# Kernel tuning notes

Hardware: AMD Instinct MI355X
Metric: run time of the kernel (lower is better)

Reference implementation:

```python
import jax, jax.numpy as jnp
import numpy as np

NUM_FEATURES = 5
HIDDEN = 64
NUM_CLASSES = 5
N_NODES = 100000
N_EDGES = 1600000


def setup_inputs() -> dict:
    key = jax.random.key(0)
    ks = jax.random.split(key, 8)
    x = jax.random.normal(ks[0], (N_NODES, 4, NUM_FEATURES), dtype=jnp.float32)
    edge_index = jax.random.randint(ks[1], (2, N_EDGES), 0, N_NODES, dtype=jnp.int64)
    batch = jnp.zeros((N_NODES,), dtype=jnp.int64)
    # GCNConv layer 1: 5 -> 64, layer 2: 64 -> 64, output Linear: 64 -> 5
    W1 = jax.random.normal(ks[2], (NUM_FEATURES, HIDDEN), dtype=jnp.float32) / np.sqrt(NUM_FEATURES)
    b1 = jnp.zeros((HIDDEN,), dtype=jnp.float32)
    W2 = jax.random.normal(ks[3], (HIDDEN, HIDDEN), dtype=jnp.float32) / np.sqrt(HIDDEN)
    b2 = jnp.zeros((HIDDEN,), dtype=jnp.float32)
    Wout = jax.random.normal(ks[4], (HIDDEN, NUM_CLASSES), dtype=jnp.float32) / np.sqrt(HIDDEN)
    bout = jnp.zeros((NUM_CLASSES,), dtype=jnp.float32)
    return {"x": x, "edge_index": edge_index, "batch": batch,
            "W1": W1, "b1": b1, "W2": W2, "b2": b2, "Wout": Wout, "bout": bout}


def reference(x, edge_index, batch, W1, b1, W2, b2, Wout, bout):
    N = x.shape[0]
    src, dst = edge_index[0], edge_index[1]
    # GCN symmetric normalization with self-loops: deg counts incoming edges + self loop
    deg = jax.ops.segment_sum(jnp.ones(src.shape, jnp.float32), dst, num_segments=N) + 1.0
    dinv_sqrt = jax.lax.rsqrt(deg)
    norm = dinv_sqrt[src] * dinv_sqrt[dst]            # [E]
    self_norm = (1.0 / deg)[:, None]                  # self-loop weight deg^-1

    def gcn_conv(h, W, b):
        h = h @ W                                     # [N, out]
        agg = jax.ops.segment_sum(h[src] * norm[:, None], dst, num_segments=N)
        return agg + h * self_norm + b

    h = jax.nn.relu(gcn_conv(x[:, -1, :], W1, b1))    # [N, HIDDEN]
    h = jax.nn.relu(gcn_conv(h, W2, b2))              # [N, HIDDEN]
    return jax.nn.softmax(h @ Wout + bout, axis=1)    # [N, 5]
```

## Files before the change

### kernel.cpp

```cpp
#include <hip/hip_runtime.h>
#include <hip/hip_fp16.h>

#define HID 64
#define NF 5
#define NC 5

#define WSH 9
#define WINN 512
#define NBMAX 256
#define SRCB 17
#define NBLK 256


__global__ __launch_bounds__(512) void k_bcount(const int* __restrict__ dst, int E, int chunk,
                                                int nb, int* __restrict__ cntmat) {
    __shared__ int cnt[NBMAX];
    int t = threadIdx.x;
    for (int i = t; i < nb; i += 512) cnt[i] = 0;
    __syncthreads();
    int c0 = blockIdx.x * chunk;
    int c1 = c0 + chunk; if (c1 > E) c1 = E;
    for (int i = c0 + t; i < c1; i += 512)
        atomicAdd(&cnt[dst[i] >> WSH], 1);
    __syncthreads();
    for (int i = t; i < nb; i += 512) cntmat[blockIdx.x * nb + i] = cnt[i];
}

__global__ __launch_bounds__(NBLK) void k_wscan(int* __restrict__ cntmat, int nb,
                                                int* __restrict__ btot) {
    __shared__ int s[NBLK];
    int b = blockIdx.x;
    int t = threadIdx.x;
    int v = cntmat[t * nb + b];
    s[t] = v;
    __syncthreads();
    for (int o = 1; o < NBLK; o <<= 1) {
        int u = (t >= o) ? s[t - o] : 0;
        __syncthreads();
        s[t] += u;
        __syncthreads();
    }
    cntmat[t * nb + b] = s[t] - v;
    if (t == NBLK - 1) btot[b] = s[t];
}

__global__ __launch_bounds__(256) void k_bscan2(const int* __restrict__ btot, int nb, int N,
                                                int* __restrict__ bbase,
                                                int* __restrict__ offsets) {
    __shared__ int s[256];
    int t = threadIdx.x;
    int v = (t < nb) ? btot[t] : 0;
    s[t] = v;
    __syncthreads();
    for (int o = 1; o < 256; o <<= 1) {
        int u = (t >= o) ? s[t - o] : 0;
        __syncthreads();
        s[t] += u;
        __syncthreads();
    }
    if (t < nb) bbase[t] = s[t] - v;
    if (t == nb - 1) { bbase[nb] = s[t]; offsets[N] = s[t]; }
}

__global__ __launch_bounds__(512) void k_bfill(const int* __restrict__ src,
                                               const int* __restrict__ dst, int E, int chunk,
                                               int nb, const int* __restrict__ bbase,
                                               const int* __restrict__ cntmat,
                                               unsigned int* __restrict__ pairbuf) {
    __shared__ int wcur[NBMAX];
    int t = threadIdx.x;
    int blk = blockIdx.x;
    for (int i = t; i < nb; i += 512)
        wcur[i] = bbase[i] + cntmat[blk * nb + i];
    __syncthreads();
    int c0 = blk * chunk;
    int c1 = c0 + chunk; if (c1 > E) c1 = E;
    for (int i = c0 + t; i < c1; i += 512) {
        int d = dst[i];
        int b = d >> WSH;
        int p = atomicAdd(&wcur[b], 1);
        pairbuf[p] = ((unsigned)(d & (WINN - 1)) << SRCB) | (unsigned)src[i];
    }
}

__global__ __launch_bounds__(WINN) void k_csr(const unsigned int* __restrict__ pairbuf,
                                              const int* __restrict__ bbase, int N,
                                              const float* __restrict__ x,
                                              int* __restrict__ offsets,
                                              int* __restrict__ csr_src,
                                              float* __restrict__ dinv,
                                              float* __restrict__ xs8) {
    int b = blockIdx.x, t = threadIdx.x;
    int winStart = b << WSH;
    int rbeg = bbase[b], rend = bbase[b + 1];
    __shared__ int deg[WINN];
    __shared__ int cur[WINN];
    __shared__ int s[WINN];
    deg[t] = 0;
    __syncthreads();
    for (int p = rbeg + t; p < rend; p += WINN)
        atomicAdd(&deg[pairbuf[p] >> SRCB], 1);
    __syncthreads();
    int v = deg[t];
    s[t] = v;
    __syncthreads();
    for (int o = 1; o < WINN; o <<= 1) {
        int u = (t >= o) ? s[t - o] : 0;
        __syncthreads();
        s[t] += u;
        __syncthreads();
    }
    int node = winStart + t;
    if (node < N) {
        int base = rbeg + s[t] - v;
        offsets[node] = base;
        cur[t] = base;
        float dv = rsqrtf((float)v + 1.0f);
        dinv[node] = dv;
        const float* xr = x + (size_t)node * (4 * NF) + 3 * NF;
        float4 v0, v1;
        v0.x = xr[0] * dv; v0.y = xr[1] * dv; v0.z = xr[2] * dv; v0.w = xr[3] * dv;
        v1.x = xr[4] * dv; v1.y = 0.f; v1.z = 0.f; v1.w = 0.f;
        float4* xp = reinterpret_cast<float4*>(xs8 + (size_t)node * 8);
        xp[0] = v0;
        xp[1] = v1;
    }
    __syncthreads();
    for (int p = rbeg + t; p < rend; p += WINN) {
        unsigned u = pairbuf[p];
        int dl = u >> SRCB;
        int sn = u & ((1u << SRCB) - 1);
        int pos = atomicAdd(&cur[dl], 1);
        csr_src[pos] = sn;
    }
}


__global__ __launch_bounds__(256) void k_aggX(const float* __restrict__ xs8,
                                              const float* __restrict__ W1,
                                              const int* __restrict__ offsets,
                                              const int* __restrict__ csr_src,
                                              const float* __restrict__ dinv,
                                              const float* __restrict__ b1,
                                              __half* __restrict__ g1, int N) {
    int wid = (blockIdx.x * blockDim.x + threadIdx.x) >> 6;
    int lane = threadIdx.x & 63;
    int g = lane >> 1;
    int h = lane & 1;
    float w0 = W1[0 * HID + lane], w1 = W1[1 * HID + lane], w2 = W1[2 * HID + lane],
          w3 = W1[3 * HID + lane], w4 = W1[4 * HID + lane];
    if (wid >= N) return;
    int e0 = offsets[wid], e1 = offsets[wid + 1];
    float4 acc = {0.f, 0.f, 0.f, 0.f};
    int ee = e0 + g;
    int s = (ee < e1) ? csr_src[ee] : -1;
    for (int e = e0; e < e1; e += 32) {
        int cs = s;
        int en = e + 32 + g;
        s = (en < e1) ? csr_src[en] : -1;
        bool p = (cs >= 0);
        int csc = p ? cs : 0;
        float4 v = *reinterpret_cast<const float4*>(xs8 + (size_t)csc * 8 + (h << 2));
        if (p) { acc.x += v.x; acc.y += v.y; acc.z += v.z; acc.w += v.w; }
    }
    if (g == 0) {
        float4 v = *reinterpret_cast<const float4*>(xs8 + (size_t)wid * 8 + (h << 2));
        acc.x += v.x; acc.y += v.y; acc.z += v.z; acc.w += v.w;
    }
#pragma unroll
    for (int o = 2; o < 64; o <<= 1) {
        acc.x += __shfl_xor(acc.x, o, 64);
        acc.y += __shfl_xor(acc.y, o, 64);
        acc.z += __shfl_xor(acc.z, o, 64);
        acc.w += __shfl_xor(acc.w, o, 64);
    }
    float a0 = __shfl(acc.x, 0, 2), a1 = __shfl(acc.y, 0, 2),
          a2 = __shfl(acc.z, 0, 2), a3 = __shfl(acc.w, 0, 2),
          a4 = __shfl(acc.x, 1, 2);
    float dv = dinv[wid];
    float sres = a0 * w0 + a1 * w1 + a2 * w2 + a3 * w3 + a4 * w4;
    float r = fmaxf(fmaf(dv, sres, b1[lane]), 0.f) * dv;
    g1[(size_t)wid * HID + lane] = __float2half(r);
}

__global__ __launch_bounds__(256) void k_aggG(const __half* __restrict__ g1,
                                              const int* __restrict__ offsets,
                                              const int* __restrict__ csr_src,
                                              const float* __restrict__ dinv,
                                              float* __restrict__ aggH, int N) {
    int wid = (blockIdx.x * blockDim.x + threadIdx.x) >> 6;
    if (wid >= N) return;
    int lane = threadIdx.x & 63;
    int g = lane >> 3;
    int f8 = (lane & 7) << 3;
    int e0 = offsets[wid], e1 = offsets[wid + 1];
    float acc[8];
#pragma unroll
    for (int i = 0; i < 8; ++i) acc[i] = 0.f;
    int ee = e0 + g;
    int s0 = (ee < e1) ? csr_src[ee] : -1;
    int s1 = (ee + 8 < e1) ? csr_src[ee + 8] : -1;
    for (int e = e0; e < e1; e += 16) {
        int cs0 = s0, cs1 = s1;
        int en0 = e + 16 + g, en1 = e + 24 + g;
        s0 = (en0 < e1) ? csr_src[en0] : -1;
        s1 = (en1 < e1) ? csr_src[en1] : -1;
        bool p0 = (cs0 >= 0), p1 = (cs1 >= 0);
        int c0 = p0 ? cs0 : 0, c1 = p1 ? cs1 : 0;
        float4 raw0 = *reinterpret_cast<const float4*>(g1 + (size_t)c0 * HID + f8);
        float4 raw1 = *reinterpret_cast<const float4*>(g1 + (size_t)c1 * HID + f8);
        if (p0) {
            float2 q0 = __half22float2(*reinterpret_cast<__half2*>(&raw0.x));
            float2 q1 = __half22float2(*reinterpret_cast<__half2*>(&raw0.y));
            float2 q2 = __half22float2(*reinterpret_cast<__half2*>(&raw0.z));
            float2 q3 = __half22float2(*reinterpret_cast<__half2*>(&raw0.w));
            acc[0] += q0.x; acc[1] += q0.y; acc[2] += q1.x; acc[3] += q1.y;
            acc[4] += q2.x; acc[5] += q2.y; acc[6] += q3.x; acc[7] += q3.y;
        }
        if (p1) {
            float2 q0 = __half22float2(*reinterpret_cast<__half2*>(&raw1.x));
            float2 q1 = __half22float2(*reinterpret_cast<__half2*>(&raw1.y));
            float2 q2 = __half22float2(*reinterpret_cast<__half2*>(&raw1.z));
            float2 q3 = __half22float2(*reinterpret_cast<__half2*>(&raw1.w));
            acc[0] += q0.x; acc[1] += q0.y; acc[2] += q1.x; acc[3] += q1.y;
            acc[4] += q2.x; acc[5] += q2.y; acc[6] += q3.x; acc[7] += q3.y;
        }
    }
#pragma unroll
    for (int o = 8; o < 64; o <<= 1) {
#pragma unroll
        for (int i = 0; i < 8; ++i) acc[i] += __shfl_xor(acc[i], o, 64);
    }
    if (lane < 8) {
        float4 raw = *reinterpret_cast<const float4*>(g1 + (size_t)wid * HID + f8);
        float2 q0 = __half22float2(*reinterpret_cast<__half2*>(&raw.x));
        float2 q1 = __half22float2(*reinterpret_cast<__half2*>(&raw.y));
        float2 q2 = __half22float2(*reinterpret_cast<__half2*>(&raw.z));
        float2 q3 = __half22float2(*reinterpret_cast<__half2*>(&raw.w));
        float dv = dinv[wid];
        float4 r0, r1;
        r0.x = dv * (acc[0] + q0.x); r0.y = dv * (acc[1] + q0.y);
        r0.z = dv * (acc[2] + q1.x); r0.w = dv * (acc[3] + q1.y);
        r1.x = dv * (acc[4] + q2.x); r1.y = dv * (acc[5] + q2.y);
        r1.z = dv * (acc[6] + q3.x); r1.w = dv * (acc[7] + q3.y);
        float4* dst4 = reinterpret_cast<float4*>(aggH + (size_t)wid * HID + f8);
        dst4[0] = r0;
        dst4[1] = r1;
    }
}

__global__ __launch_bounds__(256) void k_fuse(const float* __restrict__ aggH,
                                              const float* __restrict__ W2,
                                              const float* __restrict__ b2,
                                              const float* __restrict__ Wout,
                                              const float* __restrict__ bout,
                                              float* __restrict__ out, int N) {
    __shared__ float4 sh4[64][17];
    __shared__ float4 sW4[64 * 16];
    __shared__ float  swout[64][NC];
    __shared__ float  sb2[64];
    __shared__ float  sbout[8];
    int tx = threadIdx.x;
    int nb0 = blockIdx.x * 64;

    const float4* W2_4 = reinterpret_cast<const float4*>(W2);
    for (int i = tx; i < 64 * 16; i += 256) sW4[i] = W2_4[i];
    const float4* aggH4 = reinterpret_cast<const float4*>(aggH);
    for (int i = tx; i < 64 * 16; i += 256) {
        int row = i >> 4, c4 = i & 15;
        int node = nb0 + row;
        float4 v = {0.f, 0.f, 0.f, 0.f};
        if (node < N) v = aggH4[(size_t)node * 16 + c4];
        sh4[row][c4] = v;
    }
    if (tx < 64) sb2[tx] = b2[tx];
    for (int i = tx; i < 64 * NC; i += 256) swout[i / NC][i % NC] = Wout[i];
    if (tx < NC) sbout[tx] = bout[tx];
    __syncthreads();

    int ty = tx >> 4;
    int txl = tx & 15;

    float acc[4][4];
#pragma unroll
    for (int j = 0; j < 4; ++j)
#pragma unroll
        for (int i = 0; i < 4; ++i) acc[j][i] = 0.f;

    for (int k4 = 0; k4 < 16; ++k4) {
        float4 w0 = sW4[(k4 * 4 + 0) * 16 + txl];
        float4 w1 = sW4[(k4 * 4 + 1) * 16 + txl];
        float4 w2 = sW4[(k4 * 4 + 2) * 16 + txl];
        float4 w3 = sW4[(k4 * 4 + 3) * 16 + txl];
#pragma unroll
        for (int j = 0; j < 4; ++j) {
            float4 hq = sh4[ty * 4 + j][k4];
            acc[j][0] = fmaf(hq.x, w0.x, fmaf(hq.y, w1.x, fmaf(hq.z, w2.x, fmaf(hq.w, w3.x, acc[j][0]))));
            acc[j][1] = fmaf(hq.x, w0.y, fmaf(hq.y, w1.y, fmaf(hq.z, w2.y, fmaf(hq.w, w3.y, acc[j][1]))));
            acc[j][2] = fmaf(hq.x, w0.z, fmaf(hq.y, w1.z, fmaf(hq.z, w2.z, fmaf(hq.w, w3.z, acc[j][2]))));
            acc[j][3] = fmaf(hq.x, w0.w, fmaf(hq.y, w1.w, fmaf(hq.z, w2.w, fmaf(hq.w, w3.w, acc[j][3]))));
        }
    }

    float pl[4][NC];
#pragma unroll
    for (int j = 0; j < 4; ++j)
#pragma unroll
        for (int c = 0; c < NC; ++c) pl[j][c] = 0.f;
#pragma unroll
    for (int j = 0; j < 4; ++j) {
#pragma unroll
        for (int i = 0; i < 4; ++i) {
            int f = txl * 4 + i;
            float h2 = fmaxf(acc[j][i] + sb2[f], 0.f);
#pragma unroll
            for (int c = 0; c < NC; ++c) pl[j][c] = fmaf(h2, swout[f][c], pl[j][c]);
        }
    }
#pragma unroll
    for (int o = 1; o < 16; o <<= 1) {
#pragma unroll
        for (int j = 0; j < 4; ++j)
#pragma unroll
            for (int c = 0; c < NC; ++c) pl[j][c] += __shfl_xor(pl[j][c], o, 64);
    }
    if (txl == 0) {
#pragma unroll
        for (int j = 0; j < 4; ++j) {
            int node = nb0 + ty * 4 + j;
            if (node < N) {
                float lg[NC];
#pragma unroll
                for (int c = 0; c < NC; ++c) lg[c] = pl[j][c] + sbout[c];
                float m = lg[0];
#pragma unroll
                for (int c = 1; c < NC; ++c) m = fmaxf(m, lg[c]);
                float ssum = 0.f, ex[NC];
#pragma unroll
                for (int c = 0; c < NC; ++c) { ex[c] = __expf(lg[c] - m); ssum += ex[c]; }
                float inv = 1.0f / ssum;
#pragma unroll
                for (int c = 0; c < NC; ++c) out[(size_t)node * NC + c] = ex[c] * inv;
            }
        }
    }
}


extern "C" void kernel_launch(void* const* d_in, const int* in_sizes, int n_in,
                              void* d_out, int out_size, void* d_ws, size_t ws_size,
                              hipStream_t stream) {
    const float* x   = (const float*)d_in[0];
    const int*   ei  = (const int*)d_in[1];
    const float* W1  = (const float*)d_in[3];
    const float* b1  = (const float*)d_in[4];
    const float* W2  = (const float*)d_in[5];
    const float* b2  = (const float*)d_in[6];
    const float* Wo  = (const float*)d_in[7];
    const float* bo  = (const float*)d_in[8];
    float* out = (float*)d_out;

    const int N = in_sizes[2];
    const int E = in_sizes[1] / 2;

    size_t off = 0;
    char* base = (char*)d_ws;
    auto alloc = [&](size_t bytes) -> void* {
        off = (off + 255) & ~(size_t)255;
        void* r = base + off;
        off += bytes;
        return r;
    };
    int*      cntmat  = (int*)alloc((size_t)NBLK * NBMAX * 4);
    int*      btot    = (int*)alloc((size_t)NBMAX * 4);
    int*      bbase   = (int*)alloc(((size_t)NBMAX + 1) * 4);
    unsigned* pairbuf = (unsigned*)alloc((size_t)E * 4);
    int*      offsets = (int*)alloc(((size_t)N + 1) * 4);
    int*      csr_src = (int*)alloc((size_t)E * 4);
    float*    dinv    = (float*)alloc((size_t)N * 4);
    float*    xs8     = (float*)alloc((size_t)N * 8 * 4);
    __half*   g1      = (__half*)alloc((size_t)N * HID * 2);
    float*    aggH    = (float*)alloc((size_t)N * HID * 4);

    const int T = 256;
    int gNF = ((N * HID) + T - 1) / T;

    const int* src = ei;
    const int* dst = ei + E;

    int nb = (N + WINN - 1) >> WSH;
    int chunk = (E + NBLK - 1) / NBLK;

    k_bcount<<<NBLK, 512, 0, stream>>>(dst, E, chunk, nb, cntmat);
    k_wscan<<<nb, NBLK, 0, stream>>>(cntmat, nb, btot);
    k_bscan2<<<1, 256, 0, stream>>>(btot, nb, N, bbase, offsets);
    k_bfill<<<NBLK, 512, 0, stream>>>(src, dst, E, chunk, nb, bbase, cntmat, pairbuf);
    k_csr<<<nb, WINN, 0, stream>>>(pairbuf, bbase, N, x, offsets, csr_src, dinv, xs8);

    k_aggX<<<gNF, T, 0, stream>>>(xs8, W1, offsets, csr_src, dinv, b1, g1, N);

    k_aggG<<<gNF, T, 0, stream>>>(g1, offsets, csr_src, dinv, aggH, N);

    int nbF = (N + 63) / 64;
    k_fuse<<<nbF, 256, 0, stream>>>(aggH, W2, b2, Wo, bo, out, N);
}
```

Baseline: 209.5 us.

## Vectorize edge bucketing loads, unroll gather to 32 edges, store aggH as half

The bucket count and fill kernels now read dst and src four at a time with int4 loads, and the chunk size is rounded to a multiple of four so those loads stay aligned. The layer-2 gather loop is unrolled to keep four neighbor rows in flight per lane group instead of two. The intermediate aggregated features are stored in fp16 rather than fp32, which halves the write and read traffic between the gather and fused MLP kernels. The fp16 storage adds rounding error before the W2 matmul, and the wider unroll raises register pressure.

Result: faster. 201.7 us (-3.7%).

```diff
diff --git a/kernel.cpp b/kernel.cpp
--- a/kernel.cpp
+++ b/kernel.cpp
@@ -20,8 +20,17 @@
     __syncthreads();
     int c0 = blockIdx.x * chunk;
     int c1 = c0 + chunk; if (c1 > E) c1 = E;
-    for (int i = c0 + t; i < c1; i += 512)
-        atomicAdd(&cnt[dst[i] >> WSH], 1);
+    for (int i = c0 + t * 4; i < c1; i += 512 * 4) {
+        if (i + 3 < c1) {
+            int4 d4 = *reinterpret_cast<const int4*>(dst + i);
+            atomicAdd(&cnt[d4.x >> WSH], 1);
+            atomicAdd(&cnt[d4.y >> WSH], 1);
+            atomicAdd(&cnt[d4.z >> WSH], 1);
+            atomicAdd(&cnt[d4.w >> WSH], 1);
+        } else {
+            for (int k = i; k < c1; ++k) atomicAdd(&cnt[dst[k] >> WSH], 1);
+        }
+    }
     __syncthreads();
     for (int i = t; i < nb; i += 512) cntmat[blockIdx.x * nb + i] = cnt[i];
 }
@@ -75,11 +84,26 @@
     __syncthreads();
     int c0 = blk * chunk;
     int c1 = c0 + chunk; if (c1 > E) c1 = E;
-    for (int i = c0 + t; i < c1; i += 512) {
-        int d = dst[i];
-        int b = d >> WSH;
-        int p = atomicAdd(&wcur[b], 1);
-        pairbuf[p] = ((unsigned)(d & (WINN - 1)) << SRCB) | (unsigned)src[i];
+    for (int i = c0 + t * 4; i < c1; i += 512 * 4) {
+        if (i + 3 < c1) {
+            int4 d4 = *reinterpret_cast<const int4*>(dst + i);
+            int4 s4 = *reinterpret_cast<const int4*>(src + i);
+            int p;
+            p = atomicAdd(&wcur[d4.x >> WSH], 1);
+            pairbuf[p] = ((unsigned)(d4.x & (WINN - 1)) << SRCB) | (unsigned)s4.x;
+            p = atomicAdd(&wcur[d4.y >> WSH], 1);
+            pairbuf[p] = ((unsigned)(d4.y & (WINN - 1)) << SRCB) | (unsigned)s4.y;
+            p = atomicAdd(&wcur[d4.z >> WSH], 1);
+            pairbuf[p] = ((unsigned)(d4.z & (WINN - 1)) << SRCB) | (unsigned)s4.z;
+            p = atomicAdd(&wcur[d4.w >> WSH], 1);
+            pairbuf[p] = ((unsigned)(d4.w & (WINN - 1)) << SRCB) | (unsigned)s4.w;
+        } else {
+            for (int k = i; k < c1; ++k) {
+                int d = dst[k];
+                int p = atomicAdd(&wcur[d >> WSH], 1);
+                pairbuf[p] = ((unsigned)(d & (WINN - 1)) << SRCB) | (unsigned)src[k];
+            }
+        }
     }
 }
 
@@ -187,7 +211,7 @@
                                               const int* __restrict__ offsets,
                                               const int* __restrict__ csr_src,
                                               const float* __restrict__ dinv,
-                                              float* __restrict__ aggH, int N) {
+                                              __half* __restrict__ aggH, int N) {
     int wid = (blockIdx.x * blockDim.x + threadIdx.x) >> 6;
     if (wid >= N) return;
     int lane = threadIdx.x & 63;
@@ -200,15 +224,21 @@
     int ee = e0 + g;
     int s0 = (ee < e1) ? csr_src[ee] : -1;
     int s1 = (ee + 8 < e1) ? csr_src[ee + 8] : -1;
-    for (int e = e0; e < e1; e += 16) {
-        int cs0 = s0, cs1 = s1;
-        int en0 = e + 16 + g, en1 = e + 24 + g;
-        s0 = (en0 < e1) ? csr_src[en0] : -1;
-        s1 = (en1 < e1) ? csr_src[en1] : -1;
-        bool p0 = (cs0 >= 0), p1 = (cs1 >= 0);
-        int c0 = p0 ? cs0 : 0, c1 = p1 ? cs1 : 0;
+    int s2 = (ee + 16 < e1) ? csr_src[ee + 16] : -1;
+    int s3 = (ee + 24 < e1) ? csr_src[ee + 24] : -1;
+    for (int e = e0; e < e1; e += 32) {
+        int cs0 = s0, cs1 = s1, cs2 = s2, cs3 = s3;
+        int nb0 = e + 32 + g;
+        s0 = (nb0 < e1) ? csr_src[nb0] : -1;
+        s1 = (nb0 + 8 < e1) ? csr_src[nb0 + 8] : -1;
+        s2 = (nb0 + 16 < e1) ? csr_src[nb0 + 16] : -1;
+        s3 = (nb0 + 24 < e1) ? csr_src[nb0 + 24] : -1;
+        bool p0 = (cs0 >= 0), p1 = (cs1 >= 0), p2 = (cs2 >= 0), p3 = (cs3 >= 0);
+        int c0 = p0 ? cs0 : 0, c1 = p1 ? cs1 : 0, c2 = p2 ? cs2 : 0, c3 = p3 ? cs3 : 0;
         float4 raw0 = *reinterpret_cast<const float4*>(g1 + (size_t)c0 * HID + f8);
         float4 raw1 = *reinterpret_cast<const float4*>(g1 + (size_t)c1 * HID + f8);
+        float4 raw2 = *reinterpret_cast<const float4*>(g1 + (size_t)c2 * HID + f8);
+        float4 raw3 = *reinterpret_cast<const float4*>(g1 + (size_t)c3 * HID + f8);
         if (p0) {
             float2 q0 = __half22float2(*reinterpret_cast<__half2*>(&raw0.x));
             float2 q1 = __half22float2(*reinterpret_cast<__half2*>(&raw0.y));
@@ -225,6 +255,22 @@
             acc[0] += q0.x; acc[1] += q0.y; acc[2] += q1.x; acc[3] += q1.y;
             acc[4] += q2.x; acc[5] += q2.y; acc[6] += q3.x; acc[7] += q3.y;
         }
+        if (p2) {
+            float2 q0 = __half22float2(*reinterpret_cast<__half2*>(&raw2.x));
+            float2 q1 = __half22float2(*reinterpret_cast<__half2*>(&raw2.y));
+            float2 q2 = __half22float2(*reinterpret_cast<__half2*>(&raw2.z));
+            float2 q3 = __half22float2(*reinterpret_cast<__half2*>(&raw2.w));
+            acc[0] += q0.x; acc[1] += q0.y; acc[2] += q1.x; acc[3] += q1.y;
+            acc[4] += q2.x; acc[5] += q2.y; acc[6] += q3.x; acc[7] += q3.y;
+        }
+        if (p3) {
+            float2 q0 = __half22float2(*reinterpret_cast<__half2*>(&raw3.x));
+            float2 q1 = __half22float2(*reinterpret_cast<__half2*>(&raw3.y));
+            float2 q2 = __half22float2(*reinterpret_cast<__half2*>(&raw3.z));
+            float2 q3 = __half22float2(*reinterpret_cast<__half2*>(&raw3.w));
+            acc[0] += q0.x; acc[1] += q0.y; acc[2] += q1.x; acc[3] += q1.y;
+            acc[4] += q2.x; acc[5] += q2.y; acc[6] += q3.x; acc[7] += q3.y;
+        }
     }
 #pragma unroll
     for (int o = 8; o < 64; o <<= 1) {
@@ -238,18 +284,16 @@
         float2 q2 = __half22float2(*reinterpret_cast<__half2*>(&raw.z));
         float2 q3 = __half22float2(*reinterpret_cast<__half2*>(&raw.w));
         float dv = dinv[wid];
-        float4 r0, r1;
-        r0.x = dv * (acc[0] + q0.x); r0.y = dv * (acc[1] + q0.y);
-        r0.z = dv * (acc[2] + q1.x); r0.w = dv * (acc[3] + q1.y);
-        r1.x = dv * (acc[4] + q2.x); r1.y = dv * (acc[5] + q2.y);
-        r1.z = dv * (acc[6] + q3.x); r1.w = dv * (acc[7] + q3.y);
-        float4* dst4 = reinterpret_cast<float4*>(aggH + (size_t)wid * HID + f8);
-        dst4[0] = r0;
-        dst4[1] = r1;
-    }
-}
-
-__global__ __launch_bounds__(256) void k_fuse(const float* __restrict__ aggH,
+        float4 st;
+        *reinterpret_cast<__half2*>(&st.x) = __floats2half2_rn(dv * (acc[0] + q0.x), dv * (acc[1] + q0.y));
+        *reinterpret_cast<__half2*>(&st.y) = __floats2half2_rn(dv * (acc[2] + q1.x), dv * (acc[3] + q1.y));
+        *reinterpret_cast<__half2*>(&st.z) = __floats2half2_rn(dv * (acc[4] + q2.x), dv * (acc[5] + q2.y));
+        *reinterpret_cast<__half2*>(&st.w) = __floats2half2_rn(dv * (acc[6] + q3.x), dv * (acc[7] + q3.y));
+        *reinterpret_cast<float4*>(aggH + (size_t)wid * HID + f8) = st;
+    }
+}
+
+__global__ __launch_bounds__(256) void k_fuse(const __half* __restrict__ aggH,
                                               const float* __restrict__ W2,
                                               const float* __restrict__ b2,
                                               const float* __restrict__ Wout,
@@ -266,12 +310,17 @@
     const float4* W2_4 = reinterpret_cast<const float4*>(W2);
     for (int i = tx; i < 64 * 16; i += 256) sW4[i] = W2_4[i];
     const float4* aggH4 = reinterpret_cast<const float4*>(aggH);
-    for (int i = tx; i < 64 * 16; i += 256) {
-        int row = i >> 4, c4 = i & 15;
+    for (int i = tx; i < 64 * 8; i += 256) {
+        int row = i >> 3, h8 = i & 7;
         int node = nb0 + row;
-        float4 v = {0.f, 0.f, 0.f, 0.f};
-        if (node < N) v = aggH4[(size_t)node * 16 + c4];
-        sh4[row][c4] = v;
+        float4 raw = {0.f, 0.f, 0.f, 0.f};
+        if (node < N) raw = aggH4[(size_t)node * 8 + h8];
+        float2 q0 = __half22float2(*reinterpret_cast<__half2*>(&raw.x));
+        float2 q1 = __half22float2(*reinterpret_cast<__half2*>(&raw.y));
+        float2 q2 = __half22float2(*reinterpret_cast<__half2*>(&raw.z));
+        float2 q3 = __half22float2(*reinterpret_cast<__half2*>(&raw.w));
+        sh4[row][h8 * 2]     = make_float4(q0.x, q0.y, q1.x, q1.y);
+        sh4[row][h8 * 2 + 1] = make_float4(q2.x, q2.y, q3.x, q3.y);
     }
     if (tx < 64) sb2[tx] = b2[tx];
     for (int i = tx; i < 64 * NC; i += 256) swout[i / NC][i % NC] = Wout[i];
@@ -380,7 +429,7 @@
     float*    dinv    = (float*)alloc((size_t)N * 4);
     float*    xs8     = (float*)alloc((size_t)N * 8 * 4);
     __half*   g1      = (__half*)alloc((size_t)N * HID * 2);
-    float*    aggH    = (float*)alloc((size_t)N * HID * 4);
+    __half*   aggH    = (__half*)alloc((size_t)N * HID * 2);
 
     const int T = 256;
     int gNF = ((N * HID) + T - 1) / T;
@@ -389,7 +438,7 @@
     const int* dst = ei + E;
 
     int nb = (N + WINN - 1) >> WSH;
-    int chunk = (E + NBLK - 1) / NBLK;
+    int chunk = (((E + NBLK - 1) / NBLK) + 3) & ~3;
 
     k_bcount<<<NBLK, 512, 0, stream>>>(dst, E, chunk, nb, cntmat);
     k_wscan<<<nb, NBLK, 0, stream>>>(cntmat, nb, btot);
```
